# Kernel optimization log

Measured on AMD Instinct MI355X. Metric: run time of the kernel, lower is better.

The kernel has to match this reference:

```python
import jax, jax.numpy as jnp
import numpy as np
import math

D_MODEL = 1024
N_HEADS = 16
D_K = D_MODEL // N_HEADS
MAX_REL = 128


def setup_inputs() -> dict:
    key = jax.random.key(0)
    ks = jax.random.split(key, 10)
    B, S = 2, 2048
    std = 1.0 / math.sqrt(D_MODEL)
    inp = {
        "x": jax.random.normal(ks[0], (B, S, D_MODEL), dtype=jnp.float32),
        "Wq": jax.random.normal(ks[1], (D_MODEL, D_MODEL), dtype=jnp.float32) * std,
        "bq": jnp.zeros((D_MODEL,), dtype=jnp.float32),
        "Wk": jax.random.normal(ks[2], (D_MODEL, D_MODEL), dtype=jnp.float32) * std,
        "bk": jnp.zeros((D_MODEL,), dtype=jnp.float32),
        "Wv": jax.random.normal(ks[3], (D_MODEL, D_MODEL), dtype=jnp.float32) * std,
        "bv": jnp.zeros((D_MODEL,), dtype=jnp.float32),
        "Wo": jax.random.normal(ks[4], (D_MODEL, D_MODEL), dtype=jnp.float32) * std,
        "bo": jnp.zeros((D_MODEL,), dtype=jnp.float32),
        "rel_bias": jax.random.normal(ks[5], (N_HEADS, 2 * MAX_REL + 1), dtype=jnp.float32) * 0.02,
    }
    return inp


def _rel_bias_matrix(rel_bias, seq_len):
    # (H, S, S) gathered relative-position bias
    pos = jnp.arange(seq_len)
    rel = pos[:, None] - pos[None, :]
    idx = jnp.clip(rel, -MAX_REL, MAX_REL) + MAX_REL  # (S, S) in [0, 2M]
    return rel_bias[:, idx]  # (H, S, S)


def reference(x, Wq, bq, Wk, bk, Wv, bv, Wo, bo, rel_bias):
    B, S, _ = x.shape
    def proj(W, b):
        y = x @ W.T + b  # torch Linear: x @ W^T + b
        return y.reshape(B, S, N_HEADS, D_K).transpose(0, 2, 1, 3)  # (B,H,S,Dk)
    Q, K, V = proj(Wq, bq), proj(Wk, bk), proj(Wv, bv)
    scores = jnp.einsum("bhqd,bhkd->bhqk", Q, K) / math.sqrt(D_K)
    scores = scores + _rel_bias_matrix(rel_bias, S)[None]
    attn = jax.nn.softmax(scores, axis=-1)
    out = jnp.einsum("bhqk,bhkd->bhqd", attn, V)
    out = out.transpose(0, 2, 1, 3).reshape(B, S, D_MODEL)
    return out @ Wo.T + bo
```

## Files before the change

### kernel.cpp

```cpp
#include <hip/hip_runtime.h>

static constexpr int DM = 1024;
static constexpr int NH = 16;
static constexpr int DK = 64;
static constexpr int S  = 2048;
static constexpr int B  = 2;
static constexpr float LOG2E = 1.4426950408889634f;
static constexpr float FMAX  = 11.0f;

typedef _Float16 f16;
typedef _Float16 f16x8 __attribute__((ext_vector_type(8)));
typedef _Float16 f16x4 __attribute__((ext_vector_type(4)));
typedef __fp16   h16x2 __attribute__((ext_vector_type(2)));
typedef float    f32x4 __attribute__((ext_vector_type(4)));

static constexpr size_t NX = (size_t)B * S * DM;
static constexpr size_t NW = (size_t)DM * DM;

__global__ __launch_bounds__(256) void cvt_f16(const float* __restrict__ x,
                                               const float* __restrict__ wq,
                                               const float* __restrict__ wk,
                                               const float* __restrict__ wv,
                                               const float* __restrict__ wo,
                                               f16* __restrict__ xh,
                                               f16* __restrict__ wqh,
                                               f16* __restrict__ wkh,
                                               f16* __restrict__ wvh,
                                               f16* __restrict__ woh)
{
    const size_t base = ((size_t)blockIdx.x * 256 + threadIdx.x) * 8;
    const float* src; f16* dst; size_t off;
    if (base < NX) { src = x; dst = xh; off = base; }
    else {
        const size_t rem = base - NX;
        const int seg = (int)(rem >> 20);
        off = rem & (NW - 1);
        src = seg == 0 ? wq : (seg == 1 ? wk : (seg == 2 ? wv : wo));
        dst = seg == 0 ? wqh : (seg == 1 ? wkh : (seg == 2 ? wvh : woh));
    }
    float4 a = *(const float4*)&src[off];
    float4 b = *(const float4*)&src[off + 4];
    f16x8 h = { (f16)a.x, (f16)a.y, (f16)a.z, (f16)a.w,
                (f16)b.x, (f16)b.y, (f16)b.z, (f16)b.w };
    *(f16x8*)&dst[off] = h;
}

template<int MODE>
__global__ __launch_bounds__(256) void gemm_h(const f16* __restrict__ A,
                                              const f16* __restrict__ W0,
                                              const f16* __restrict__ W1,
                                              const f16* __restrict__ W2,
                                              const float* __restrict__ b0,
                                              const float* __restrict__ b1,
                                              const float* __restrict__ b2,
                                              void* __restrict__ o0,
                                              void* __restrict__ o1,
                                              void* __restrict__ o2)
{
    __shared__ f16 As[128 * 72];
    __shared__ f16 Bs[128 * 72];

    const int t    = threadIdx.x;
    const int w    = t >> 6;
    const int lane = t & 63;
    const int tx   = lane & 15;
    const int quad = lane >> 4;
    const int wm   = w >> 1;
    const int wn   = w & 1;
    const int m0   = blockIdx.y * 128;

    const f16* W; const float* bias; f16* outh = nullptr; float* outf = nullptr;
    float scale; int n0;
    if (MODE == 0) {
        const int wsel = blockIdx.x >> 3;
        n0   = (blockIdx.x & 7) * 128;
        W    = wsel == 0 ? W0 : (wsel == 1 ? W1 : W2);
        bias = wsel == 0 ? b0 : (wsel == 1 ? b1 : b2);
        outh = (f16*)(wsel == 0 ? o0 : (wsel == 1 ? o1 : o2));
        scale = wsel == 0 ? LOG2E * 0.125f : 1.0f;
    } else {
        n0 = blockIdx.x * 128;
        W = W0; bias = b0; outf = (float*)o0; scale = 1.0f;
    }

    const int lr = t >> 2;
    const int lc = (t & 3) * 8;

    f32x4 acc[4][4];
#pragma unroll
    for (int mt = 0; mt < 4; ++mt)
#pragma unroll
        for (int nt = 0; nt < 4; ++nt) acc[mt][nt] = (f32x4){0.f, 0.f, 0.f, 0.f};

    f16x8 ga[4], gb[4];
    {
        const f16* Ap = A + (size_t)(m0 + lr) * DM + lc;
        const f16* Wp = W + (size_t)(n0 + lr) * DM + lc;
        ga[0] = *(const f16x8*)(Ap);
        ga[1] = *(const f16x8*)(Ap + 32);
        ga[2] = *(const f16x8*)(Ap + (size_t)64 * DM);
        ga[3] = *(const f16x8*)(Ap + (size_t)64 * DM + 32);
        gb[0] = *(const f16x8*)(Wp);
        gb[1] = *(const f16x8*)(Wp + 32);
        gb[2] = *(const f16x8*)(Wp + (size_t)64 * DM);
        gb[3] = *(const f16x8*)(Wp + (size_t)64 * DM + 32);
    }

    for (int k0 = 0; k0 < DM; k0 += 64) {
        __syncthreads();
        *(f16x8*)&As[ lr       * 72 + lc     ] = ga[0];
        *(f16x8*)&As[ lr       * 72 + lc + 32] = ga[1];
        *(f16x8*)&As[(lr + 64) * 72 + lc     ] = ga[2];
        *(f16x8*)&As[(lr + 64) * 72 + lc + 32] = ga[3];
        *(f16x8*)&Bs[ lr       * 72 + lc     ] = gb[0];
        *(f16x8*)&Bs[ lr       * 72 + lc + 32] = gb[1];
        *(f16x8*)&Bs[(lr + 64) * 72 + lc     ] = gb[2];
        *(f16x8*)&Bs[(lr + 64) * 72 + lc + 32] = gb[3];
        if (k0 + 64 < DM) {
            const f16* Ap = A + (size_t)(m0 + lr) * DM + k0 + 64 + lc;
            const f16* Wp = W + (size_t)(n0 + lr) * DM + k0 + 64 + lc;
            ga[0] = *(const f16x8*)(Ap);
            ga[1] = *(const f16x8*)(Ap + 32);
            ga[2] = *(const f16x8*)(Ap + (size_t)64 * DM);
            ga[3] = *(const f16x8*)(Ap + (size_t)64 * DM + 32);
            gb[0] = *(const f16x8*)(Wp);
            gb[1] = *(const f16x8*)(Wp + 32);
            gb[2] = *(const f16x8*)(Wp + (size_t)64 * DM);
            gb[3] = *(const f16x8*)(Wp + (size_t)64 * DM + 32);
        }
        __syncthreads();

        f16x8 af[4][2];
#pragma unroll
        for (int mt = 0; mt < 4; ++mt)
#pragma unroll
            for (int ks = 0; ks < 2; ++ks)
                af[mt][ks] = *(const f16x8*)&As[(wm*64 + mt*16 + tx)*72 + ks*32 + quad*8];
#pragma unroll
        for (int nt = 0; nt < 4; ++nt) {
#pragma unroll
            for (int ks = 0; ks < 2; ++ks) {
                f16x8 bf = *(const f16x8*)&Bs[(wn*64 + nt*16 + tx)*72 + ks*32 + quad*8];
#pragma unroll
                for (int mt = 0; mt < 4; ++mt)
                    acc[mt][nt] = __builtin_amdgcn_mfma_f32_16x16x32_f16(af[mt][ks], bf, acc[mt][nt], 0, 0, 0);
            }
        }
    }

#pragma unroll
    for (int nt = 0; nt < 4; ++nt) {
        const int n = n0 + wn*64 + nt*16 + tx;
        const float bn = bias[n];
#pragma unroll
        for (int mt = 0; mt < 4; ++mt)
#pragma unroll
            for (int r = 0; r < 4; ++r) {
                const int m = m0 + wm*64 + mt*16 + quad*4 + r;
                const float v = (acc[mt][nt][r] + bn) * scale;
                if (MODE == 0) {
                    const int bi = m >> 11;
                    const int ss = m & (S - 1);
                    const int h  = n >> 6;
                    const int dk = n & (DK - 1);
                    outh[((size_t)((bi*NH + h)*S + ss))*DK + dk] = (f16)v;
                } else {
                    outf[(size_t)m * DM + n] = v;
                }
            }
    }
}

__global__ __launch_bounds__(256, 4) void attn_v5(const f16* __restrict__ Q,
                                                  const f16* __restrict__ K,
                                                  const f16* __restrict__ V,
                                                  const float* __restrict__ relb,
                                                  f16* __restrict__ aout)
{
    __shared__ f16 Ks[2 * 64*72];
    __shared__ f16 Vt[2 * 64*72];
    __shared__ float rb2[257];

    const int t    = threadIdx.x;
    const int w    = t >> 6;
    const int lane = t & 63;
    const int tx   = lane & 15;
    const int quad = lane >> 4;
    const int q0   = blockIdx.x * 128;
    const int h    = blockIdx.y;
    const int b    = blockIdx.z;

    const f16* Qb = Q + (size_t)((b*NH + h) * S) * DK;
    const f16* Kb = K + (size_t)((b*NH + h) * S) * DK;
    const f16* Vb = V + (size_t)((b*NH + h) * S) * DK;

    for (int i = t; i < 257; i += 256) rb2[i] = relb[h*257 + i] * LOG2E - FMAX;

    const int qrow = q0 + w*32 + tx;
    f16x8 qf[2][2];
#pragma unroll
    for (int qb = 0; qb < 2; ++qb)
#pragma unroll
        for (int ks = 0; ks < 2; ++ks)
            qf[qb][ks] = *(const f16x8*)(Qb + (size_t)(qrow + qb*16)*DK + ks*32 + quad*8);

    f32x4 oT[4][2];
    float lsum[2] = {0.f, 0.f};
#pragma unroll
    for (int d = 0; d < 4; ++d)
#pragma unroll
        for (int qb = 0; qb < 2; ++qb) oT[d][qb] = (f32x4){0.f, 0.f, 0.f, 0.f};

    const int seq = t & 63, d0k = (t >> 6) * 16;
    const int s2 = (t & 31) * 2, d0v = (t >> 5) * 8;
    const int g = ((s2 >> 2) & 3)*16 + (s2 >> 4)*4 + (s2 & 3);

    f16x8 kr0 = *(const f16x8*)(Kb + (size_t)seq*DK + d0k);
    f16x8 kr1 = *(const f16x8*)(Kb + (size_t)seq*DK + d0k + 8);
    f16x8 vr0 = *(const f16x8*)(Vb + (size_t)s2*DK + d0v);
    f16x8 vr1 = *(const f16x8*)(Vb + (size_t)(s2 + 1)*DK + d0v);

    for (int kt = 0; kt < S/64; ++kt) {
        const int k0 = kt * 64;
        const int db = (kt & 1) * 4608;
        f16* KsW = &Ks[db];
        f16* VtW = &Vt[db];

        *(f16x8*)&KsW[seq*72 + d0k    ] = kr0;
        *(f16x8*)&KsW[seq*72 + d0k + 8] = kr1;
        {
            const unsigned short* u0 = (const unsigned short*)&vr0;
            const unsigned short* u1 = (const unsigned short*)&vr1;
#pragma unroll
            for (int j = 0; j < 8; ++j) {
                unsigned int pw = (unsigned int)u0[j] | ((unsigned int)u1[j] << 16);
                *(unsigned int*)&VtW[(d0v + j)*72 + g] = pw;
            }
        }
        __syncthreads();

        if (kt + 1 < S/64) {
            const int k0n = k0 + 64;
            kr0 = *(const f16x8*)(Kb + (size_t)(k0n + seq)*DK + d0k);
            kr1 = *(const f16x8*)(Kb + (size_t)(k0n + seq)*DK + d0k + 8);
            vr0 = *(const f16x8*)(Vb + (size_t)(k0n + s2    )*DK + d0v);
            vr1 = *(const f16x8*)(Vb + (size_t)(k0n + s2 + 1)*DK + d0v);
        }

        const bool farlo = (k0 - q0) >= 256;
        const bool farhi = (q0 - k0) >= 192;
        const float bconst = farlo ? rb2[0] : rb2[256];
        const int relbase = (q0 + w*32 + tx) - (k0 + quad*4);

        f16x4 pf[4][2];
#pragma unroll
        for (int sb = 0; sb < 4; ++sb) {
            f32x4 sT[2];
            if (farlo | farhi) {
                sT[0] = (f32x4){bconst, bconst, bconst, bconst};
                sT[1] = sT[0];
            } else {
#pragma unroll
                for (int qb = 0; qb < 2; ++qb)
#pragma unroll
                    for (int r = 0; r < 4; ++r) {
                        int rel = relbase + qb*16 - sb*16 - r;
                        rel = rel < -128 ? -128 : (rel > 128 ? 128 : rel);
                        sT[qb][r] = rb2[rel + 128];
                    }
            }
#pragma unroll
            for (int ks = 0; ks < 2; ++ks) {
                f16x8 kf = *(const f16x8*)&KsW[(sb*16 + tx)*72 + ks*32 + quad*8];
#pragma unroll
                for (int qb = 0; qb < 2; ++qb)
                    sT[qb] = __builtin_amdgcn_mfma_f32_16x16x32_f16(kf, qf[qb][ks], sT[qb], 0, 0, 0);
            }
#pragma unroll
            for (int qb = 0; qb < 2; ++qb) {
                const float p0 = exp2f(sT[qb][0]);
                const float p1 = exp2f(sT[qb][1]);
                const float p2 = exp2f(sT[qb][2]);
                const float p3 = exp2f(sT[qb][3]);
                lsum[qb] += (p0 + p1) + (p2 + p3);
                h16x2 lo = __builtin_amdgcn_cvt_pkrtz(p0, p1);
                h16x2 hi = __builtin_amdgcn_cvt_pkrtz(p2, p3);
                pf[sb][qb] = (f16x4){ (f16)lo.x, (f16)lo.y, (f16)hi.x, (f16)hi.y };
            }
        }

#pragma unroll
        for (int d = 0; d < 4; ++d) {
#pragma unroll
            for (int sp2 = 0; sp2 < 2; ++sp2) {
                f16x8 vv = *(const f16x8*)&VtW[(d*16 + tx)*72 + quad*16 + sp2*8];
                f16x4 vlo = __builtin_shufflevector(vv, vv, 0, 1, 2, 3);
                f16x4 vhi = __builtin_shufflevector(vv, vv, 4, 5, 6, 7);
#pragma unroll
                for (int qb = 0; qb < 2; ++qb) {
                    oT[d][qb] = __builtin_amdgcn_mfma_f32_16x16x16f16(vlo, pf[sp2*2    ][qb], oT[d][qb], 0, 0, 0);
                    oT[d][qb] = __builtin_amdgcn_mfma_f32_16x16x16f16(vhi, pf[sp2*2 + 1][qb], oT[d][qb], 0, 0, 0);
                }
            }
        }
    }

#pragma unroll
    for (int qb = 0; qb < 2; ++qb) {
        float l = lsum[qb];
        l += __shfl_xor(l, 16);
        l += __shfl_xor(l, 32);
        const float inv = 1.0f / l;
        const int q = q0 + w*32 + qb*16 + tx;
#pragma unroll
        for (int d = 0; d < 4; ++d) {
            h16x2 e0 = __builtin_amdgcn_cvt_pkrtz(oT[d][qb][0]*inv, oT[d][qb][1]*inv);
            h16x2 e1 = __builtin_amdgcn_cvt_pkrtz(oT[d][qb][2]*inv, oT[d][qb][3]*inv);
            f16x4 hv = { (f16)e0.x, (f16)e0.y, (f16)e1.x, (f16)e1.y };
            *(f16x4*)&aout[((size_t)(b*S + q))*DM + h*DK + d*16 + quad*4] = hv;
        }
    }
}

extern "C" void kernel_launch(void* const* d_in, const int* in_sizes, int n_in,
                              void* d_out, int out_size, void* d_ws, size_t ws_size,
                              hipStream_t stream)
{
    const float* x    = (const float*)d_in[0];
    const float* Wq   = (const float*)d_in[1];
    const float* bq   = (const float*)d_in[2];
    const float* Wk   = (const float*)d_in[3];
    const float* bk   = (const float*)d_in[4];
    const float* Wv   = (const float*)d_in[5];
    const float* bv   = (const float*)d_in[6];
    const float* Wo   = (const float*)d_in[7];
    const float* bo   = (const float*)d_in[8];
    const float* relb = (const float*)d_in[9];

    f16* Xh  = (f16*)d_ws;
    f16* Wqh = Xh  + NX;
    f16* Wkh = Wqh + NW;
    f16* Wvh = Wkh + NW;
    f16* Woh = Wvh + NW;
    f16* Qh  = Woh + NW;
    f16* Kh  = Qh  + NX;
    f16* Vh  = Kh  + NX;
    f16* AOh = Vh  + NX;

    cvt_f16<<<(NX + 4*NW) / (256*8), 256, 0, stream>>>(x, Wq, Wk, Wv, Wo,
                                                       Xh, Wqh, Wkh, Wvh, Woh);
    gemm_h<0><<<dim3(24, 32), 256, 0, stream>>>(Xh, Wqh, Wkh, Wvh,
                                                bq, bk, bv, Qh, Kh, Vh);
    attn_v5<<<dim3(S/128, NH, B), 256, 0, stream>>>(Qh, Kh, Vh, relb, AOh);
    gemm_h<1><<<dim3(8, 32), 256, 0, stream>>>(AOh, Woh, nullptr, nullptr,
                                               bo, nullptr, nullptr,
                                               d_out, nullptr, nullptr);
}
```

Before: 235.4 us.

## Split attention KV range across two blocks and add a combine kernel

```diff
diff --git a/kernel.cpp b/kernel.cpp
--- a/kernel.cpp
+++ b/kernel.cpp
@@ -7,6 +7,7 @@
 static constexpr int B  = 2;
 static constexpr float LOG2E = 1.4426950408889634f;
 static constexpr float FMAX  = 11.0f;
+static constexpr int NSPLIT = 2;
 
 typedef _Float16 f16;
 typedef _Float16 f16x8 __attribute__((ext_vector_type(8)));
@@ -171,11 +172,12 @@
     }
 }
 
-__global__ __launch_bounds__(256, 4) void attn_v5(const f16* __restrict__ Q,
+__global__ __launch_bounds__(256, 4) void attn_v6(const f16* __restrict__ Q,
                                                   const f16* __restrict__ K,
                                                   const f16* __restrict__ V,
                                                   const float* __restrict__ relb,
-                                                  f16* __restrict__ aout)
+                                                  f16* __restrict__ On,
+                                                  float* __restrict__ lp)
 {
     __shared__ f16 Ks[2 * 64*72];
     __shared__ f16 Vt[2 * 64*72];
@@ -186,9 +188,11 @@
     const int lane = t & 63;
     const int tx   = lane & 15;
     const int quad = lane >> 4;
-    const int q0   = blockIdx.x * 128;
+    const int qt   = blockIdx.x >> 1;
+    const int sp   = blockIdx.x & 1;
     const int h    = blockIdx.y;
     const int b    = blockIdx.z;
+    const int q0   = qt * 128;
 
     const f16* Qb = Q + (size_t)((b*NH + h) * S) * DK;
     const f16* Kb = K + (size_t)((b*NH + h) * S) * DK;
@@ -215,12 +219,15 @@
     const int s2 = (t & 31) * 2, d0v = (t >> 5) * 8;
     const int g = ((s2 >> 2) & 3)*16 + (s2 >> 4)*4 + (s2 & 3);
 
-    f16x8 kr0 = *(const f16x8*)(Kb + (size_t)seq*DK + d0k);
-    f16x8 kr1 = *(const f16x8*)(Kb + (size_t)seq*DK + d0k + 8);
-    f16x8 vr0 = *(const f16x8*)(Vb + (size_t)s2*DK + d0v);
-    f16x8 vr1 = *(const f16x8*)(Vb + (size_t)(s2 + 1)*DK + d0v);
-
-    for (int kt = 0; kt < S/64; ++kt) {
+    const int kt0 = sp * (S / 64 / NSPLIT);
+    const int ktend = kt0 + S / 64 / NSPLIT;
+
+    f16x8 kr0 = *(const f16x8*)(Kb + (size_t)(kt0*64 + seq)*DK + d0k);
+    f16x8 kr1 = *(const f16x8*)(Kb + (size_t)(kt0*64 + seq)*DK + d0k + 8);
+    f16x8 vr0 = *(const f16x8*)(Vb + (size_t)(kt0*64 + s2    )*DK + d0v);
+    f16x8 vr1 = *(const f16x8*)(Vb + (size_t)(kt0*64 + s2 + 1)*DK + d0v);
+
+    for (int kt = kt0; kt < ktend; ++kt) {
         const int k0 = kt * 64;
         const int db = (kt & 1) * 4608;
         f16* KsW = &Ks[db];
@@ -239,7 +246,7 @@
         }
         __syncthreads();
 
-        if (kt + 1 < S/64) {
+        if (kt + 1 < ktend) {
             const int k0n = k0 + 64;
             kr0 = *(const f16x8*)(Kb + (size_t)(k0n + seq)*DK + d0k);
             kr1 = *(const f16x8*)(Kb + (size_t)(k0n + seq)*DK + d0k + 8);
@@ -310,16 +317,47 @@
         float l = lsum[qb];
         l += __shfl_xor(l, 16);
         l += __shfl_xor(l, 32);
-        const float inv = 1.0f / l;
         const int q = q0 + w*32 + qb*16 + tx;
+        if (quad == 0)
+            lp[(((size_t)sp*B + b)*NH + h)*S + q] = l;
 #pragma unroll
         for (int d = 0; d < 4; ++d) {
-            h16x2 e0 = __builtin_amdgcn_cvt_pkrtz(oT[d][qb][0]*inv, oT[d][qb][1]*inv);
-            h16x2 e1 = __builtin_amdgcn_cvt_pkrtz(oT[d][qb][2]*inv, oT[d][qb][3]*inv);
+            h16x2 e0 = __builtin_amdgcn_cvt_pkrtz(oT[d][qb][0], oT[d][qb][1]);
+            h16x2 e1 = __builtin_amdgcn_cvt_pkrtz(oT[d][qb][2], oT[d][qb][3]);
             f16x4 hv = { (f16)e0.x, (f16)e0.y, (f16)e1.x, (f16)e1.y };
-            *(f16x4*)&aout[((size_t)(b*S + q))*DM + h*DK + d*16 + quad*4] = hv;
-        }
-    }
+            *(f16x4*)&On[(size_t)sp*NX + ((size_t)(b*S + q))*DM + h*DK + d*16 + quad*4] = hv;
+        }
+    }
+}
+
+__global__ __launch_bounds__(256) void combine(const f16* __restrict__ On,
+                                               const float* __restrict__ lp,
+                                               f16* __restrict__ AOh)
+{
+    const size_t i8 = ((size_t)blockIdx.x * 256 + threadIdx.x) * 8;
+    const int token = (int)(i8 >> 10);
+    const int c     = (int)(i8 & (DM - 1));
+    const int b     = token >> 11;
+    const int st    = token & (S - 1);
+    const int h     = c >> 6;
+    float l = 0.f;
+#pragma unroll
+    for (int sp = 0; sp < NSPLIT; ++sp)
+        l += lp[(((size_t)sp*B + b)*NH + h)*S + st];
+    const float inv = 1.0f / l;
+    float acc[8];
+#pragma unroll
+    for (int j = 0; j < 8; ++j) acc[j] = 0.f;
+#pragma unroll
+    for (int sp = 0; sp < NSPLIT; ++sp) {
+        f16x8 v = *(const f16x8*)&On[(size_t)sp*NX + i8];
+#pragma unroll
+        for (int j = 0; j < 8; ++j) acc[j] += (float)v[j];
+    }
+    f16x8 o;
+#pragma unroll
+    for (int j = 0; j < 8; ++j) o[j] = (f16)(acc[j] * inv);
+    *(f16x8*)&AOh[i8] = o;
 }
 
 extern "C" void kernel_launch(void* const* d_in, const int* in_sizes, int n_in,
@@ -346,12 +384,15 @@
     f16* Kh  = Qh  + NX;
     f16* Vh  = Kh  + NX;
     f16* AOh = Vh  + NX;
+    f16* On  = AOh + NX;
+    float* lpart = (float*)(On + (size_t)NSPLIT*NX);
 
     cvt_f16<<<(NX + 4*NW) / (256*8), 256, 0, stream>>>(x, Wq, Wk, Wv, Wo,
                                                        Xh, Wqh, Wkh, Wvh, Woh);
     gemm_h<0><<<dim3(24, 32), 256, 0, stream>>>(Xh, Wqh, Wkh, Wvh,
                                                 bq, bk, bv, Qh, Kh, Vh);
-    attn_v5<<<dim3(S/128, NH, B), 256, 0, stream>>>(Qh, Kh, Vh, relb, AOh);
+    attn_v6<<<dim3((S/128)*NSPLIT, NH, B), 256, 0, stream>>>(Qh, Kh, Vh, relb, On, lpart);
+    combine<<<NX / (256*8), 256, 0, stream>>>(On, lpart, AOh);
     gemm_h<1><<<dim3(8, 32), 256, 0, stream>>>(AOh, Woh, nullptr, nullptr,
                                                bo, nullptr, nullptr,
                                                d_out, nullptr, nullptr);
```

Measured after the change: 221.8 us. 5.7% less time.
